# Optimization experiments

Hardware: AMD Instinct MI355X
Metric: run time of the kernel (lower is better)

## Reference

```python
import jax, jax.numpy as jnp
import numpy as np


def setup_inputs() -> dict:
    key = jax.random.key(0)
    k1, _ = jax.random.split(key)
    x = jax.random.normal(k1, (8, 128, 56, 56), dtype=jnp.float32)
    gamma = jnp.array(0.5, dtype=jnp.float32)  # learned scalar (init gamma=0.5)
    return {"x": x, "gamma": gamma}


def reference(x, gamma):
    # conv=False path: query/key/value convs are Identity, so Q=K=V=x flattened.
    B, C, H, W = x.shape
    N = H * W
    v = x.reshape(B, C, N)                          # [B, C, N]
    # energy[b, i, j] = sum_c x[b, c, i] * x[b, c, j]  (Q^T K)
    energy = jnp.einsum('bci,bcj->bij', v, v)       # [B, N, N]
    # multiplicative mask: zero out the diagonal BEFORE softmax (not -inf)
    mask = 1.0 - jnp.eye(N, dtype=energy.dtype)
    attention = jax.nn.softmax(energy * mask, axis=-1)  # [B, N, N]
    # out = bmm(V, attention): out[b, c, j] = sum_i v[b, c, i] * attention[b, i, j]
    out = jnp.einsum('bci,bij->bcj', v, attention)  # [B, C, N]
    out = jax.nn.relu(out).reshape(B, C, H, W)
    y = gamma * out + x
    return (y, out, x, gamma)
```

## Files before the change

### kernel.cpp

```cpp
#include <hip/hip_runtime.h>
#include <math.h>

#define Bb 8
#define Cc 128
#define Nn 3136
#define Np 3200
#define NT 50
#define Mm (Bb*Cc*Nn)
#define PADV 72
#define L2E 1.44269504088896340736f
#define C44 (44.0f * L2E)

#define XT2B (NT*16*64*8)
#define TSZA (16*64*8)
#define XC2B (NT*8*128*8)
#define TSZV (8*128*8)

typedef unsigned short u16;
typedef unsigned int   u32;
typedef __attribute__((ext_vector_type(8)))  u16      u16x8;
typedef __attribute__((ext_vector_type(8)))  _Float16 f16x8;
typedef __attribute__((ext_vector_type(4)))  _Float16 f16x4;
typedef __attribute__((ext_vector_type(4)))  float    f32x4;
typedef __attribute__((ext_vector_type(16))) float    f32x16;

__device__ __forceinline__ float exp2fast(float x) {
#if __has_builtin(__builtin_amdgcn_exp2f)
    return __builtin_amdgcn_exp2f(x);
#else
    float r; asm("v_exp_f32 %0, %1" : "=v"(r) : "v"(x)); return r;
#endif
}

typedef __attribute__((address_space(1))) const unsigned int gas_u32;
typedef __attribute__((address_space(3))) unsigned int las_u32;
__device__ __forceinline__ void gload_lds16(const u16* g, u16* l) {
    __builtin_amdgcn_global_load_lds((gas_u32*)g, (las_u32*)l, 16, 0, 0);
}

__global__ __launch_bounds__(256) void prep_kernel(const float* __restrict__ x,
                                                   const float* __restrict__ gamma_p,
                                                   float* __restrict__ out,
                                                   u16* __restrict__ xt2,
                                                   u16* __restrict__ xc2,
                                                   float* __restrict__ row_d) {
    const int bx = blockIdx.x;
    const int b = bx / 50, nblk = bx % 50;
    const int t = threadIdx.x;

    if (nblk == 49) {
        const u16x8 z8 = {0, 0, 0, 0, 0, 0, 0, 0};
        u16* dt = xt2 + ((size_t)b * NT + 49) * TSZA;
        u16* dc = xc2 + ((size_t)b * NT + 49) * TSZV;
        #pragma unroll
        for (int it = 0; it < 4; ++it) {
            *(u16x8*)&dt[(it * 256 + t) * 8] = z8;
            *(u16x8*)&dc[(it * 256 + t) * 8] = z8;
        }
        if (t < 64) row_d[b * Np + Nn + t] = 1.0f;
        return;
    }

    __shared__ float lx[Cc][65];
    const int n0 = nblk * 64;

    #pragma unroll 8
    for (int r = 0; r < 32; ++r) {
        const int c = r * 4 + (t >> 6);
        const int g = (b * Cc + c) * Nn + n0 + (t & 63);
        lx[c][t & 63] = x[g];
    }
    __syncthreads();

    {
        const int nl = t & 63, cseg = t >> 6;
        u16x8 hv[4];
        #pragma unroll
        for (int cc = 0; cc < 32; ++cc) {
            const _Float16 hh = (_Float16)lx[cseg * 32 + cc][nl];
            hv[cc >> 3][cc & 7] = __builtin_bit_cast(u16, hh);
        }
        u16* base = xt2 + (((size_t)(b * NT + nblk) * 16 + cseg * 4) * 64 + nl) * 8;
        #pragma unroll
        for (int k = 0; k < 4; ++k) *(u16x8*)&base[k * (64 * 8)] = hv[k];
    }
    {
        const int c = t >> 1, half = t & 1;
        u16x8 hv[4];
        #pragma unroll
        for (int k = 0; k < 32; ++k) {
            const _Float16 hh = (_Float16)lx[c][half * 32 + k];
            hv[k >> 3][k & 7] = __builtin_bit_cast(u16, hh);
        }
        u16* base = xc2 + (((size_t)(b * NT + nblk) * 8 + half * 4) * 128 + c) * 8;
        #pragma unroll
        for (int k = 0; k < 4; ++k) *(u16x8*)&base[k * (128 * 8)] = hv[k];
    }
    if (bx == 0 && t == 0) out[(size_t)3 * Mm] = gamma_p[0];
}

__global__ __launch_bounds__(256, 4) void stats_kernel(const u16* __restrict__ xt2,
                                                       float* __restrict__ row_d) {
    __shared__ __align__(16) u16 s_j[2][TSZA];

    const int bx = blockIdx.x;
    const int b = bx & 7, rem = bx >> 3;
    const int i0t = rem >> 3, jq = rem & 7;
    const int t = threadIdx.x;
    const int w = t >> 6, l = t & 63, lane = l & 31, h = l >> 5;
    const int igrp = w & 1, jsub = w >> 1;
    const u16* __restrict__ xb = xt2 + (size_t)b * XT2B;

    f16x8 Bf[8];
    const int irow = igrp * 32 + lane;
    #pragma unroll
    for (int kk = 0; kk < 8; ++kk)
        Bf[kk] = *(const f16x8*)&xb[(((size_t)i0t * 16 + 2 * kk + h) * 64 + irow) * 8];

    const int jt0 = jq * 6 + (jq < 2 ? jq : 2);
    const int jcnt = 6 + (jq < 2 ? 1 : 0);
    const int jrow = jsub * 32 + lane;
    const int wsh = w * 2048;

    {
        const u16* gs = xb + (size_t)jt0 * TSZA + wsh + l * 8;
        u16* ls = &s_j[0][wsh];
        #pragma unroll
        for (int k = 0; k < 4; ++k) gload_lds16(gs + k * 512, ls + k * 512);
    }
    __syncthreads();

    float sa = 0.f, sb = 0.f;
    for (int jt = jt0; jt < jt0 + jcnt; ++jt) {
        const int cur = (jt - jt0) & 1;
        if (jt + 1 < jt0 + jcnt) {
            const u16* gs = xb + (size_t)(jt + 1) * TSZA + wsh + l * 8;
            u16* ls = &s_j[cur ^ 1][wsh];
            #pragma unroll
            for (int k = 0; k < 4; ++k) gload_lds16(gs + k * 512, ls + k * 512);
        }

        const u16* sj = &s_j[cur][0];
        f32x16 ea, eb;
        #pragma unroll
        for (int r = 0; r < 16; ++r) { ea[r] = 0.f; eb[r] = 0.f; }
        __builtin_amdgcn_s_setprio(1);
        #pragma unroll
        for (int kk = 0; kk < 4; ++kk) {
            const f16x8 A0 = *(const f16x8*)&sj[((4 * kk + h) * 64 + jrow) * 8];
            const f16x8 A1 = *(const f16x8*)&sj[((4 * kk + 2 + h) * 64 + jrow) * 8];
            ea = __builtin_amdgcn_mfma_f32_32x32x16_f16(A0, Bf[2 * kk],     ea, 0, 0, 0);
            eb = __builtin_amdgcn_mfma_f32_32x32x16_f16(A1, Bf[2 * kk + 1], eb, 0, 0, 0);
        }
        __builtin_amdgcn_s_setprio(0);

        if (jt == i0t) {
            const bool dsub = (jsub == igrp);
            #pragma unroll
            for (int r = 0; r < 16; ++r) {
                const int mrow = (r & 3) + 8 * (r >> 2) + 4 * h;
                float v = ea[r] + eb[r];
                if (dsub && mrow == lane) v = 0.f;
                const float e = exp2fast(fmaf(v, L2E, -C44));
                if (r & 1) sb += e; else sa += e;
            }
        } else {
            #pragma unroll
            for (int r = 0; r < 16; ++r) {
                const float e = exp2fast(fmaf(ea[r] + eb[r], L2E, -C44));
                if (r & 1) sb += e; else sa += e;
            }
        }
        __syncthreads();
    }
    float ssum = sa + sb;
    ssum += __shfl_xor(ssum, 32, 64);
    if (h == 0) atomicAdd(&row_d[b * Np + i0t * 64 + igrp * 32 + lane], ssum);
}

__global__ __launch_bounds__(256) void conv_kernel(float* __restrict__ row_d) {
    const int i = blockIdx.x * 256 + threadIdx.x;
    row_d[i] = C44 + __log2f(row_d[i]);
}

__global__ __launch_bounds__(256, 2) void out_kernel(const u16* __restrict__ xt2,
                                                     const u16* __restrict__ xc2,
                                                     const float* __restrict__ row_c,
                                                     float* __restrict__ out) {
    __shared__ __align__(16) u16 s_xa[2][TSZA];
    __shared__ __align__(16) u16 s_xv[2][TSZV];
    __shared__ __align__(16) u16 s_pt[64 * PADV];

    const int bx = blockIdx.x;
    const int b = bx & 7, rem = bx >> 3;
    const int j0t = rem >> 1, ih = rem & 1;
    const int ti0 = ih * 25, ti1 = ti0 + 25;
    const int t = threadIdx.x;
    const int w = t >> 6, l = t & 63, lane = l & 31, h = l >> 5;
    const int isub = w & 1, jgrp = w >> 1;
    const int jg = w & 1,  cp = w >> 1;
    const u16* __restrict__ xtb = xt2 + (size_t)b * XT2B;
    const u16* __restrict__ xcb = xc2 + (size_t)b * XC2B;

    f16x8 Bj[8];
    const int jrow = jgrp * 32 + lane;
    #pragma unroll
    for (int kk = 0; kk < 8; ++kk)
        Bj[kk] = *(const f16x8*)&xtb[(((size_t)j0t * 16 + 2 * kk + h) * 64 + jrow) * 8];

    f32x16 oa, ob;
    #pragma unroll
    for (int r = 0; r < 16; ++r) { oa[r] = 0.f; ob[r] = 0.f; }

    const int arow = isub * 32 + lane;
    const int ptbase = (jgrp * 32 + lane) * PADV + isub * 32;
    const int pbrow = (jg * 32 + lane) * PADV + h * 8;

    const bool wA = (w < 2);
    const int sh = (w & 1) * 4096;

    {
        const u16* gs = (wA ? xtb + (size_t)ti0 * TSZA : xcb + (size_t)ti0 * TSZV)
                        + sh + l * 8;
        u16* ls = (wA ? &s_xa[0][0] : &s_xv[0][0]) + sh;
        #pragma unroll
        for (int k = 0; k < 8; ++k) gload_lds16(gs + k * 512, ls + k * 512);
    }
    __syncthreads();

    for (int ti = ti0; ti < ti1; ++ti) {
        const int cur = (ti - ti0) & 1;
        if (ti + 1 < ti1) {
            const u16* gs = (wA ? xtb + (size_t)(ti + 1) * TSZA
                                : xcb + (size_t)(ti + 1) * TSZV) + sh + l * 8;
            u16* ls = (wA ? &s_xa[cur ^ 1][0] : &s_xv[cur ^ 1][0]) + sh;
            #pragma unroll
            for (int k = 0; k < 8; ++k) gload_lds16(gs + k * 512, ls + k * 512);
        }

        const u16* sa = &s_xa[cur][0];
        f32x16 ea;
        #pragma unroll
        for (int r = 0; r < 16; ++r) ea[r] = 0.f;
        __builtin_amdgcn_s_setprio(1);
        #pragma unroll
        for (int kk = 0; kk < 8; ++kk) {
            const f16x8 A = *(const f16x8*)&sa[((2 * kk + h) * 64 + arow) * 8];
            ea = __builtin_amdgcn_mfma_f32_32x32x16_f16(A, Bj[kk], ea, 0, 0, 0);
        }
        __builtin_amdgcn_s_setprio(0);

        const float* cbase = &row_c[b * Np + ti * 64 + isub * 32];
        if (ti == j0t) {
            const bool dsub = (isub == jgrp);
            #pragma unroll
            for (int qq = 0; qq < 4; ++qq) {
                const f32x4 cv = *(const f32x4*)&cbase[qq * 8 + h * 4];
                f16x4 pv;
                #pragma unroll
                for (int r = 0; r < 4; ++r) {
                    const int m = qq * 8 + h * 4 + r;
                    float v = ea[qq * 4 + r];
                    if (dsub && m == lane) v = 0.f;
                    pv[r] = (_Float16)exp2fast(fmaf(v, L2E, -cv[r]));
                }
                *(f16x4*)&s_pt[ptbase + qq * 8 + h * 4] = pv;
            }
        } else {
            #pragma unroll
            for (int qq = 0; qq < 4; ++qq) {
                const f32x4 cv = *(const f32x4*)&cbase[qq * 8 + h * 4];
                f16x4 pv;
                #pragma unroll
                for (int r = 0; r < 4; ++r)
                    pv[r] = (_Float16)exp2fast(fmaf(ea[qq * 4 + r], L2E, -cv[r]));
                *(f16x4*)&s_pt[ptbase + qq * 8 + h * 4] = pv;
            }
        }
        __syncthreads();

        const u16* sv = &s_xv[cur][0];
        __builtin_amdgcn_s_setprio(1);
        #pragma unroll
        for (int kk = 0; kk < 4; ++kk) {
            const f16x8 Bp  = *(const f16x8*)&s_pt[pbrow + kk * 16];
            const f16x8 Av0 = *(const f16x8*)&sv[((2 * kk + h) * 128 + cp * 64 + lane) * 8];
            const f16x8 Av1 = *(const f16x8*)&sv[((2 * kk + h) * 128 + cp * 64 + 32 + lane) * 8];
            oa = __builtin_amdgcn_mfma_f32_32x32x16_f16(Av0, Bp, oa, 0, 0, 0);
            ob = __builtin_amdgcn_mfma_f32_32x32x16_f16(Av1, Bp, ob, 0, 0, 0);
        }
        __builtin_amdgcn_s_setprio(0);
        __syncthreads();
    }

    #pragma unroll
    for (int r = 0; r < 16; ++r) {
        const int mrow = (r & 3) + 8 * (r >> 2) + 4 * h;
        const int jj = j0t * 64 + jg * 32 + lane;
        {
            const int c = cp * 64 + mrow;
            const size_t pos = (size_t)(b * Cc + c) * Nn + jj;
            out[(size_t)ih * Mm + pos] = oa[r];
        }
        {
            const int c = cp * 64 + 32 + mrow;
            const size_t pos = (size_t)(b * Cc + c) * Nn + jj;
            out[(size_t)ih * Mm + pos] = ob[r];
        }
    }
}

__global__ __launch_bounds__(256) void finish_kernel(const float* __restrict__ x,
                                                     const float* __restrict__ gamma_p,
                                                     float* __restrict__ out) {
    const float gamma = gamma_p[0];
    const size_t base = ((size_t)blockIdx.x * 256 + threadIdx.x) * 4;
    const f32x4 pa = *(const f32x4*)&out[base];
    const f32x4 pb = *(const f32x4*)&out[(size_t)Mm + base];
    const f32x4 xv = *(const f32x4*)&x[base];
    f32x4 yo, oo;
    #pragma unroll
    for (int r = 0; r < 4; ++r) {
        const float o = fmaxf(pa[r] + pb[r], 0.0f);
        oo[r] = o;
        yo[r] = fmaf(gamma, o, xv[r]);
    }
    *(f32x4*)&out[base] = yo;
    *(f32x4*)&out[(size_t)Mm + base] = oo;
    *(f32x4*)&out[(size_t)2 * Mm + base] = xv;
}

extern "C" void kernel_launch(void* const* d_in, const int* in_sizes, int n_in,
                              void* d_out, int out_size, void* d_ws, size_t ws_size,
                              hipStream_t stream) {
    const float* x       = (const float*)d_in[0];
    const float* gamma_p = (const float*)d_in[1];
    float* out = (float*)d_out;

    float* row_d = (float*)d_ws;
    u16* xt2 = (u16*)((char*)d_ws + (1 << 17));
    u16* xc2 = xt2 + (size_t)Bb * XT2B;

    hipMemsetAsync(row_d, 0, (size_t)Bb * Np * sizeof(float), stream);
    prep_kernel  <<<400, 256, 0, stream>>>(x, gamma_p, out, xt2, xc2, row_d);
    stats_kernel <<<3136, 256, 0, stream>>>(xt2, row_d);
    conv_kernel  <<<100, 256, 0, stream>>>(row_d);
    out_kernel   <<<784, 256, 0, stream>>>(xt2, xc2, row_d, out);
    finish_kernel<<<3136, 256, 0, stream>>>(x, gamma_p, out);
}
```

Before: 191.6 us.

## Process two row tiles per block in stats and out kernels with triple-buffered loads

The stats kernel now gives each block two i-tiles (ip and ip+25), so each loaded j tile feeds twice the MFMA work. It also moves from double to triple buffering with explicit waitcnt and barriers. The out kernel handles two j-tiles per block and splits the i range three ways instead of two, so finish_kernel now sums three partial outputs. This reduces LDS and global traffic per unit of work, at the cost of more registers, fewer blocks, a lower occupancy bound, and one more partial buffer read in finish.

```diff
diff --git a/kernel.cpp b/kernel.cpp
--- a/kernel.cpp
+++ b/kernel.cpp
@@ -38,6 +38,12 @@
     __builtin_amdgcn_global_load_lds((gas_u32*)g, (las_u32*)l, 16, 0, 0);
 }
 
+#define BAR()    __builtin_amdgcn_s_barrier()
+#define SCHED0() __builtin_amdgcn_sched_barrier(0)
+#define W_LGKM() asm volatile("s_waitcnt lgkmcnt(0)" ::: "memory")
+#define W_ALL()  asm volatile("s_waitcnt vmcnt(0) lgkmcnt(0)" ::: "memory")
+#define W_VM4()  asm volatile("s_waitcnt vmcnt(4) lgkmcnt(0)" ::: "memory")
+
 __global__ __launch_bounds__(256) void prep_kernel(const float* __restrict__ x,
                                                    const float* __restrict__ gamma_p,
                                                    float* __restrict__ out,
@@ -99,23 +105,28 @@
     if (bx == 0 && t == 0) out[(size_t)3 * Mm] = gamma_p[0];
 }
 
-__global__ __launch_bounds__(256, 4) void stats_kernel(const u16* __restrict__ xt2,
+__global__ __launch_bounds__(256, 3) void stats_kernel(const u16* __restrict__ xt2,
                                                        float* __restrict__ row_d) {
-    __shared__ __align__(16) u16 s_j[2][TSZA];
+    __shared__ __align__(16) u16 s_j[3][TSZA];
 
     const int bx = blockIdx.x;
     const int b = bx & 7, rem = bx >> 3;
-    const int i0t = rem >> 3, jq = rem & 7;
+    const int ip = rem >> 3, jq = rem & 7;
+    const int itA = ip, itB = ip + 25;
     const int t = threadIdx.x;
     const int w = t >> 6, l = t & 63, lane = l & 31, h = l >> 5;
     const int igrp = w & 1, jsub = w >> 1;
     const u16* __restrict__ xb = xt2 + (size_t)b * XT2B;
 
-    f16x8 Bf[8];
+    f16x8 Bf[2][8];
     const int irow = igrp * 32 + lane;
     #pragma unroll
-    for (int kk = 0; kk < 8; ++kk)
-        Bf[kk] = *(const f16x8*)&xb[(((size_t)i0t * 16 + 2 * kk + h) * 64 + irow) * 8];
+    for (int s = 0; s < 2; ++s) {
+        const int it = s ? itB : itA;
+        #pragma unroll
+        for (int kk = 0; kk < 8; ++kk)
+            Bf[s][kk] = *(const f16x8*)&xb[(((size_t)it * 16 + 2 * kk + h) * 64 + irow) * 8];
+    }
 
     const int jt0 = jq * 6 + (jq < 2 ? jq : 2);
     const int jcnt = 6 + (jq < 2 ? 1 : 0);
@@ -128,54 +139,65 @@
         #pragma unroll
         for (int k = 0; k < 4; ++k) gload_lds16(gs + k * 512, ls + k * 512);
     }
-    __syncthreads();
-
-    float sa = 0.f, sb = 0.f;
-    for (int jt = jt0; jt < jt0 + jcnt; ++jt) {
-        const int cur = (jt - jt0) & 1;
-        if (jt + 1 < jt0 + jcnt) {
-            const u16* gs = xb + (size_t)(jt + 1) * TSZA + wsh + l * 8;
-            u16* ls = &s_j[cur ^ 1][wsh];
-            #pragma unroll
-            for (int k = 0; k < 4; ++k) gload_lds16(gs + k * 512, ls + k * 512);
+    if (jcnt > 1) {
+        const u16* gs = xb + (size_t)(jt0 + 1) * TSZA + wsh + l * 8;
+        u16* ls = &s_j[1][wsh];
+        #pragma unroll
+        for (int k = 0; k < 4; ++k) gload_lds16(gs + k * 512, ls + k * 512);
+        W_VM4();
+    } else {
+        W_ALL();
+    }
+    BAR(); SCHED0();
+
+    float sA = 0.f, sB = 0.f;
+    for (int k = 0; k < jcnt; ++k) {
+        const int jt = jt0 + k, cur = k % 3;
+        const bool more = (k + 2 < jcnt);
+        if (more) {
+            const u16* gs = xb + (size_t)(jt + 2) * TSZA + wsh + l * 8;
+            u16* ls = &s_j[(k + 2) % 3][wsh];
+            #pragma unroll
+            for (int kq = 0; kq < 4; ++kq) gload_lds16(gs + kq * 512, ls + kq * 512);
         }
 
         const u16* sj = &s_j[cur][0];
-        f32x16 ea, eb;
-        #pragma unroll
-        for (int r = 0; r < 16; ++r) { ea[r] = 0.f; eb[r] = 0.f; }
-        __builtin_amdgcn_s_setprio(1);
-        #pragma unroll
-        for (int kk = 0; kk < 4; ++kk) {
-            const f16x8 A0 = *(const f16x8*)&sj[((4 * kk + h) * 64 + jrow) * 8];
-            const f16x8 A1 = *(const f16x8*)&sj[((4 * kk + 2 + h) * 64 + jrow) * 8];
-            ea = __builtin_amdgcn_mfma_f32_32x32x16_f16(A0, Bf[2 * kk],     ea, 0, 0, 0);
-            eb = __builtin_amdgcn_mfma_f32_32x32x16_f16(A1, Bf[2 * kk + 1], eb, 0, 0, 0);
-        }
-        __builtin_amdgcn_s_setprio(0);
-
-        if (jt == i0t) {
-            const bool dsub = (jsub == igrp);
+        #pragma unroll
+        for (int s = 0; s < 2; ++s) {
+            f32x16 ea, eb;
+            #pragma unroll
+            for (int r = 0; r < 16; ++r) { ea[r] = 0.f; eb[r] = 0.f; }
+            __builtin_amdgcn_s_setprio(1);
+            #pragma unroll
+            for (int kk = 0; kk < 4; ++kk) {
+                const f16x8 A0 = *(const f16x8*)&sj[((4 * kk + h) * 64 + jrow) * 8];
+                const f16x8 A1 = *(const f16x8*)&sj[((4 * kk + 2 + h) * 64 + jrow) * 8];
+                ea = __builtin_amdgcn_mfma_f32_32x32x16_f16(A0, Bf[s][2 * kk],     ea, 0, 0, 0);
+                eb = __builtin_amdgcn_mfma_f32_32x32x16_f16(A1, Bf[s][2 * kk + 1], eb, 0, 0, 0);
+            }
+            __builtin_amdgcn_s_setprio(0);
+
+            float acc = 0.f;
+            const bool diag = (jt == (s ? itB : itA)) && (jsub == igrp);
             #pragma unroll
             for (int r = 0; r < 16; ++r) {
                 const int mrow = (r & 3) + 8 * (r >> 2) + 4 * h;
                 float v = ea[r] + eb[r];
-                if (dsub && mrow == lane) v = 0.f;
-                const float e = exp2fast(fmaf(v, L2E, -C44));
-                if (r & 1) sb += e; else sa += e;
-            }
-        } else {
-            #pragma unroll
-            for (int r = 0; r < 16; ++r) {
-                const float e = exp2fast(fmaf(ea[r] + eb[r], L2E, -C44));
-                if (r & 1) sb += e; else sa += e;
-            }
-        }
-        __syncthreads();
-    }
-    float ssum = sa + sb;
-    ssum += __shfl_xor(ssum, 32, 64);
-    if (h == 0) atomicAdd(&row_d[b * Np + i0t * 64 + igrp * 32 + lane], ssum);
+                if (diag && mrow == lane) v = 0.f;
+                acc += exp2fast(fmaf(v, L2E, -C44));
+            }
+            if (s) sB += acc; else sA += acc;
+        }
+
+        if (more) { W_VM4(); } else { W_ALL(); }
+        BAR(); SCHED0();
+    }
+    sA += __shfl_xor(sA, 32, 64);
+    sB += __shfl_xor(sB, 32, 64);
+    if (h == 0) {
+        atomicAdd(&row_d[b * Np + itA * 64 + igrp * 32 + lane], sA);
+        atomicAdd(&row_d[b * Np + itB * 64 + igrp * 32 + lane], sB);
+    }
 }
 
 __global__ __launch_bounds__(256) void conv_kernel(float* __restrict__ row_d) {
@@ -193,8 +215,10 @@
 
     const int bx = blockIdx.x;
     const int b = bx & 7, rem = bx >> 3;
-    const int j0t = rem >> 1, ih = rem & 1;
-    const int ti0 = ih * 25, ti1 = ti0 + 25;
+    const int jp = rem / 3, q = rem % 3;
+    const int jtA = 2 * jp, jtB = 2 * jp + 1;
+    const int ti0 = q * 17;
+    const int ti1 = (q == 2) ? 50 : ti0 + 17;
     const int t = threadIdx.x;
     const int w = t >> 6, l = t & 63, lane = l & 31, h = l >> 5;
     const int isub = w & 1, jgrp = w >> 1;
@@ -202,15 +226,19 @@
     const u16* __restrict__ xtb = xt2 + (size_t)b * XT2B;
     const u16* __restrict__ xcb = xc2 + (size_t)b * XC2B;
 
-    f16x8 Bj[8];
+    f16x8 Bj[2][8];
     const int jrow = jgrp * 32 + lane;
     #pragma unroll
-    for (int kk = 0; kk < 8; ++kk)
-        Bj[kk] = *(const f16x8*)&xtb[(((size_t)j0t * 16 + 2 * kk + h) * 64 + jrow) * 8];
-
-    f32x16 oa, ob;
-    #pragma unroll
-    for (int r = 0; r < 16; ++r) { oa[r] = 0.f; ob[r] = 0.f; }
+    for (int s = 0; s < 2; ++s) {
+        const int jt = s ? jtB : jtA;
+        #pragma unroll
+        for (int kk = 0; kk < 8; ++kk)
+            Bj[s][kk] = *(const f16x8*)&xtb[(((size_t)jt * 16 + 2 * kk + h) * 64 + jrow) * 8];
+    }
+
+    f32x16 aA0, aA1, aB0, aB1;
+    #pragma unroll
+    for (int r = 0; r < 16; ++r) { aA0[r] = 0.f; aA1[r] = 0.f; aB0[r] = 0.f; aB1[r] = 0.f; }
 
     const int arow = isub * 32 + lane;
     const int ptbase = (jgrp * 32 + lane) * PADV + isub * 32;
@@ -237,22 +265,24 @@
             #pragma unroll
             for (int k = 0; k < 8; ++k) gload_lds16(gs + k * 512, ls + k * 512);
         }
-
         const u16* sa = &s_xa[cur][0];
-        f32x16 ea;
-        #pragma unroll
-        for (int r = 0; r < 16; ++r) ea[r] = 0.f;
-        __builtin_amdgcn_s_setprio(1);
-        #pragma unroll
-        for (int kk = 0; kk < 8; ++kk) {
-            const f16x8 A = *(const f16x8*)&sa[((2 * kk + h) * 64 + arow) * 8];
-            ea = __builtin_amdgcn_mfma_f32_32x32x16_f16(A, Bj[kk], ea, 0, 0, 0);
-        }
-        __builtin_amdgcn_s_setprio(0);
-
+        const u16* sv = &s_xv[cur][0];
         const float* cbase = &row_c[b * Np + ti * 64 + isub * 32];
-        if (ti == j0t) {
-            const bool dsub = (isub == jgrp);
+
+        #pragma unroll
+        for (int s = 0; s < 2; ++s) {
+            f32x16 ea;
+            #pragma unroll
+            for (int r = 0; r < 16; ++r) ea[r] = 0.f;
+            __builtin_amdgcn_s_setprio(1);
+            #pragma unroll
+            for (int kk = 0; kk < 8; ++kk) {
+                const f16x8 A = *(const f16x8*)&sa[((2 * kk + h) * 64 + arow) * 8];
+                ea = __builtin_amdgcn_mfma_f32_32x32x16_f16(A, Bj[s][kk], ea, 0, 0, 0);
+            }
+            __builtin_amdgcn_s_setprio(0);
+
+            const bool dsub = (ti == (s ? jtB : jtA)) && (isub == jgrp);
             #pragma unroll
             for (int qq = 0; qq < 4; ++qq) {
                 const f32x4 cv = *(const f32x4*)&cbase[qq * 8 + h * 4];
@@ -266,46 +296,47 @@
                 }
                 *(f16x4*)&s_pt[ptbase + qq * 8 + h * 4] = pv;
             }
-        } else {
-            #pragma unroll
-            for (int qq = 0; qq < 4; ++qq) {
-                const f32x4 cv = *(const f32x4*)&cbase[qq * 8 + h * 4];
-                f16x4 pv;
-                #pragma unroll
-                for (int r = 0; r < 4; ++r)
-                    pv[r] = (_Float16)exp2fast(fmaf(ea[qq * 4 + r], L2E, -cv[r]));
-                *(f16x4*)&s_pt[ptbase + qq * 8 + h * 4] = pv;
-            }
-        }
-        __syncthreads();
-
-        const u16* sv = &s_xv[cur][0];
-        __builtin_amdgcn_s_setprio(1);
-        #pragma unroll
-        for (int kk = 0; kk < 4; ++kk) {
-            const f16x8 Bp  = *(const f16x8*)&s_pt[pbrow + kk * 16];
-            const f16x8 Av0 = *(const f16x8*)&sv[((2 * kk + h) * 128 + cp * 64 + lane) * 8];
-            const f16x8 Av1 = *(const f16x8*)&sv[((2 * kk + h) * 128 + cp * 64 + 32 + lane) * 8];
-            oa = __builtin_amdgcn_mfma_f32_32x32x16_f16(Av0, Bp, oa, 0, 0, 0);
-            ob = __builtin_amdgcn_mfma_f32_32x32x16_f16(Av1, Bp, ob, 0, 0, 0);
-        }
-        __builtin_amdgcn_s_setprio(0);
-        __syncthreads();
+            W_LGKM(); BAR(); SCHED0();
+
+            __builtin_amdgcn_s_setprio(1);
+            #pragma unroll
+            for (int kk = 0; kk < 4; ++kk) {
+                const f16x8 Bp  = *(const f16x8*)&s_pt[pbrow + kk * 16];
+                const f16x8 Av0 = *(const f16x8*)&sv[((2 * kk + h) * 128 + cp * 64 + lane) * 8];
+                const f16x8 Av1 = *(const f16x8*)&sv[((2 * kk + h) * 128 + cp * 64 + 32 + lane) * 8];
+                if (s) {
+                    aB0 = __builtin_amdgcn_mfma_f32_32x32x16_f16(Av0, Bp, aB0, 0, 0, 0);
+                    aB1 = __builtin_amdgcn_mfma_f32_32x32x16_f16(Av1, Bp, aB1, 0, 0, 0);
+                } else {
+                    aA0 = __builtin_amdgcn_mfma_f32_32x32x16_f16(Av0, Bp, aA0, 0, 0, 0);
+                    aA1 = __builtin_amdgcn_mfma_f32_32x32x16_f16(Av1, Bp, aA1, 0, 0, 0);
+                }
+            }
+            __builtin_amdgcn_s_setprio(0);
+
+            if (s == 0) { W_LGKM(); BAR(); SCHED0(); }
+        }
+
+        if (ti + 1 < ti1) { W_ALL(); } else { W_LGKM(); }
+        BAR(); SCHED0();
     }
 
     #pragma unroll
     for (int r = 0; r < 16; ++r) {
         const int mrow = (r & 3) + 8 * (r >> 2) + 4 * h;
-        const int jj = j0t * 64 + jg * 32 + lane;
         {
-            const int c = cp * 64 + mrow;
-            const size_t pos = (size_t)(b * Cc + c) * Nn + jj;
-            out[(size_t)ih * Mm + pos] = oa[r];
-        }
-        {
-            const int c = cp * 64 + 32 + mrow;
-            const size_t pos = (size_t)(b * Cc + c) * Nn + jj;
-            out[(size_t)ih * Mm + pos] = ob[r];
+            const int jj = jtA * 64 + jg * 32 + lane;
+            const size_t p0 = (size_t)(b * Cc + cp * 64 + mrow) * Nn + jj;
+            const size_t p1 = (size_t)(b * Cc + cp * 64 + 32 + mrow) * Nn + jj;
+            out[(size_t)q * Mm + p0] = aA0[r];
+            out[(size_t)q * Mm + p1] = aA1[r];
+        }
+        if (jtB < 49) {
+            const int jj = jtB * 64 + jg * 32 + lane;
+            const size_t p0 = (size_t)(b * Cc + cp * 64 + mrow) * Nn + jj;
+            const size_t p1 = (size_t)(b * Cc + cp * 64 + 32 + mrow) * Nn + jj;
+            out[(size_t)q * Mm + p0] = aB0[r];
+            out[(size_t)q * Mm + p1] = aB1[r];
         }
     }
 }
@@ -317,11 +348,12 @@
     const size_t base = ((size_t)blockIdx.x * 256 + threadIdx.x) * 4;
     const f32x4 pa = *(const f32x4*)&out[base];
     const f32x4 pb = *(const f32x4*)&out[(size_t)Mm + base];
+    const f32x4 pc = *(const f32x4*)&out[(size_t)2 * Mm + base];
     const f32x4 xv = *(const f32x4*)&x[base];
     f32x4 yo, oo;
     #pragma unroll
     for (int r = 0; r < 4; ++r) {
-        const float o = fmaxf(pa[r] + pb[r], 0.0f);
+        const float o = fmaxf(pa[r] + pb[r] + pc[r], 0.0f);
         oo[r] = o;
         yo[r] = fmaf(gamma, o, xv[r]);
     }
@@ -343,8 +375,8 @@
 
     hipMemsetAsync(row_d, 0, (size_t)Bb * Np * sizeof(float), stream);
     prep_kernel  <<<400, 256, 0, stream>>>(x, gamma_p, out, xt2, xc2, row_d);
-    stats_kernel <<<3136, 256, 0, stream>>>(xt2, row_d);
+    stats_kernel <<<1600, 256, 0, stream>>>(xt2, row_d);
     conv_kernel  <<<100, 256, 0, stream>>>(row_d);
-    out_kernel   <<<784, 256, 0, stream>>>(xt2, xc2, row_d, out);
+    out_kernel   <<<600, 256, 0, stream>>>(xt2, xc2, row_d, out);
     finish_kernel<<<3136, 256, 0, stream>>>(x, gamma_p, out);
 }
```

Measured after the change: 191.4 us. No clear change (-0.1%).
